# Performance work log

Measured on AMD Instinct MI355X. Metric: run time of the kernel, lower is better.

The kernel has to match this reference:

```python
import jax, jax.numpy as jnp
import numpy as np

N_NODES = 100000
N_EDGES = 1250000
D_FEAT = 64


def setup_inputs() -> dict:
    key = jax.random.key(0)
    kx, ke = jax.random.split(key)
    x = jax.random.normal(kx, (N_NODES, D_FEAT), dtype=jnp.float32)
    edge_index = jax.random.randint(ke, (2, N_EDGES), 0, N_NODES, dtype=jnp.int64)
    return {"x": x, "edge_index": edge_index}


def reference(x, edge_index):
    # adj[src, dst] = 1; x_neighbors = adj.T @ x  ->
    # x_neighbors[i] = sum_{edges (s, d) with d == i} x[s]
    src, dst = edge_index[0], edge_index[1]
    msgs = x[src]  # [n_edges, d_feat] gather
    x_neighbors = jax.ops.segment_sum(msgs, dst, num_segments=x.shape[0])
    return x_neighbors
```

## Files before the change

kernel.cpp:

```cpp
#include <hip/hip_runtime.h>
#include <hip/hip_bf16.h>

#define N_NODES 100000
#define N_EDGES 1250000
#define D_FEAT  64
#define SB_NODES 512
#define SB_SHIFT 9
#define NSB     196
#define CAP_SB  7040
#define OVF_CAP 8192
#define EPB_I4  1024
#define N_I4    (N_EDGES / 4)
#define NBLK_BUILD ((N_I4 + EPB_I4 - 1) / EPB_I4)
#define RT      512

__global__ __launch_bounds__(256) void to_bf16(
    const float* __restrict__ x, ushort* __restrict__ xh, uint* __restrict__ fill)
{
    if (blockIdx.x == 0) {
        for (int i = threadIdx.x; i < NSB + 2; i += 256) fill[i] = 0u;
    }
    int t = blockIdx.x * 256 + threadIdx.x;
    const float4* x4 = (const float4*)x;
    float4 a = x4[2 * t];
    float4 b = x4[2 * t + 1];
    float f[8] = {a.x, a.y, a.z, a.w, b.x, b.y, b.z, b.w};
    uint h[8];
#pragma unroll
    for (int i = 0; i < 8; ++i) {
        uint u = __float_as_uint(f[i]);
        u += 0x7FFFu + ((u >> 16) & 1u);
        h[i] = u >> 16;
    }
    uint4 o;
    o.x = h[0] | (h[1] << 16);
    o.y = h[2] | (h[3] << 16);
    o.z = h[4] | (h[5] << 16);
    o.w = h[6] | (h[7] << 16);
    ((uint4*)xh)[t] = o;
}

__global__ __launch_bounds__(256) void build_sb(
    const int* __restrict__ src, const int* __restrict__ dst,
    uint* __restrict__ fill, uint* __restrict__ pairs,
    uint* __restrict__ ovfCnt, int2* __restrict__ ovf)
{
    __shared__ uint cnt[NSB];
    __shared__ uint base[NSB];
    const int t = threadIdx.x;
    for (int i = t; i < NSB; i += 256) cnt[i] = 0;
    __syncthreads();

    uint   pw[16];
    ushort pb[16];
    ushort pr[16];
    bool   vk[4];
    const int i40 = blockIdx.x * EPB_I4;
#pragma unroll
    for (int k = 0; k < 4; ++k) {
        int i4 = i40 + t + k * 256;
        vk[k] = (i4 < N_I4);
        if (vk[k]) {
            int4 d4 = ((const int4*)dst)[i4];
            int4 s4 = ((const int4*)src)[i4];
            int dd[4] = {d4.x, d4.y, d4.z, d4.w};
            int ss[4] = {s4.x, s4.y, s4.z, s4.w};
#pragma unroll
            for (int j = 0; j < 4; ++j) {
                uint b = ((uint)dd[j]) >> SB_SHIFT;
                uint r = atomicAdd(&cnt[b], 1u);
                pw[k * 4 + j] = ((((uint)dd[j]) & (SB_NODES - 1u)) << 17) | (uint)ss[j];
                pb[k * 4 + j] = (ushort)b;
                pr[k * 4 + j] = (ushort)r;
            }
        }
    }
    __syncthreads();

    for (int i = t; i < NSB; i += 256) {
        uint c = cnt[i];
        base[i] = c ? atomicAdd(&fill[i], c) : 0u;
    }
    __syncthreads();

#pragma unroll
    for (int j = 0; j < 16; ++j) {
        if (vk[j >> 2]) {
            uint b = pb[j];
            uint g = base[b] + pr[j];
            if (g < CAP_SB) {
                pairs[(size_t)b * CAP_SB + g] = pw[j];
            } else {
                uint o = atomicAdd(ovfCnt, 1u);
                if (o < OVF_CAP)
                    ovf[o] = make_int2((int)(pw[j] & 0x1FFFFu),
                                       (int)((b << SB_SHIFT) | (pw[j] >> 17)));
            }
        }
    }
}

__global__ __launch_bounds__(RT) void repart(
    uint* __restrict__ pairs, const uint* __restrict__ fill,
    uint* __restrict__ offs)
{
    __shared__ uint pw[CAP_SB];
    __shared__ int  cnt[SB_NODES];
    __shared__ int  scn[SB_NODES];
    __shared__ int  pos[SB_NODES];

    const int t  = threadIdx.x;
    const int sb = blockIdx.x;
    const int n  = min((int)fill[sb], CAP_SB);
    const size_t base = (size_t)sb * CAP_SB;

    cnt[t] = 0;
    __syncthreads();
    for (int i = t; i < n; i += RT) {
        uint w = pairs[base + i];
        pw[i] = w;
        atomicAdd(&cnt[w >> 17], 1);
    }
    __syncthreads();

    scn[t] = cnt[t];
    __syncthreads();
    for (int off = 1; off < SB_NODES; off <<= 1) {
        int v = (t >= off) ? scn[t - off] : 0;
        __syncthreads();
        scn[t] += v;
        __syncthreads();
    }
    {
        int e = scn[t] - cnt[t];
        pos[t] = e;
        offs[sb * SB_NODES + t] = (uint)e | ((uint)cnt[t] << 16);
    }
    __syncthreads();

    for (int i = t; i < n; i += RT) {
        uint w = pw[i];
        int r = atomicAdd(&pos[w >> 17], 1);
        pairs[base + r] = w & 0x1FFFFu;
    }
}

__global__ __launch_bounds__(256) void gather_csr(
    const ushort* __restrict__ xh, const uint* __restrict__ pairs,
    const uint* __restrict__ offs, const float* __restrict__ x,
    const int2* __restrict__ ovf, const uint* __restrict__ ovfCnt,
    float* __restrict__ out)
{
    const int t    = threadIdx.x;
    const int lane = t & 63;
    const int sub  = lane >> 3;
    const int l8   = lane & 7;
    const int node = blockIdx.x * 4 + (t >> 6);
    if (node >= N_NODES) return;
    const uint4* __restrict__ xrow = (const uint4*)xh;

    const uint v    = offs[node];
    const int start = (node >> SB_SHIFT) * CAP_SB + (int)(v & 0xFFFFu);
    const int deg   = (int)(v >> 16);

    float f[8];
#pragma unroll
    for (int j = 0; j < 8; ++j) f[j] = 0.f;

    int i = sub;
    for (; i + 8 < deg; i += 16) {
        uint s0 = pairs[start + i];
        uint s1 = pairs[start + i + 8];
        uint4 v0 = xrow[(size_t)s0 * 8 + l8];
        uint4 v1 = xrow[(size_t)s1 * 8 + l8];
        f[0] += __uint_as_float((v0.x & 0xFFFFu) << 16);
        f[1] += __uint_as_float(v0.x & 0xFFFF0000u);
        f[2] += __uint_as_float((v0.y & 0xFFFFu) << 16);
        f[3] += __uint_as_float(v0.y & 0xFFFF0000u);
        f[4] += __uint_as_float((v0.z & 0xFFFFu) << 16);
        f[5] += __uint_as_float(v0.z & 0xFFFF0000u);
        f[6] += __uint_as_float((v0.w & 0xFFFFu) << 16);
        f[7] += __uint_as_float(v0.w & 0xFFFF0000u);
        f[0] += __uint_as_float((v1.x & 0xFFFFu) << 16);
        f[1] += __uint_as_float(v1.x & 0xFFFF0000u);
        f[2] += __uint_as_float((v1.y & 0xFFFFu) << 16);
        f[3] += __uint_as_float(v1.y & 0xFFFF0000u);
        f[4] += __uint_as_float((v1.z & 0xFFFFu) << 16);
        f[5] += __uint_as_float(v1.z & 0xFFFF0000u);
        f[6] += __uint_as_float((v1.w & 0xFFFFu) << 16);
        f[7] += __uint_as_float(v1.w & 0xFFFF0000u);
    }
    if (i < deg) {
        uint s0 = pairs[start + i];
        uint4 v0 = xrow[(size_t)s0 * 8 + l8];
        f[0] += __uint_as_float((v0.x & 0xFFFFu) << 16);
        f[1] += __uint_as_float(v0.x & 0xFFFF0000u);
        f[2] += __uint_as_float((v0.y & 0xFFFFu) << 16);
        f[3] += __uint_as_float(v0.y & 0xFFFF0000u);
        f[4] += __uint_as_float((v0.z & 0xFFFFu) << 16);
        f[5] += __uint_as_float(v0.z & 0xFFFF0000u);
        f[6] += __uint_as_float((v0.w & 0xFFFFu) << 16);
        f[7] += __uint_as_float(v0.w & 0xFFFF0000u);
    }

#pragma unroll
    for (int j = 0; j < 8; ++j) {
        f[j] += __shfl_xor(f[j], 8, 64);
        f[j] += __shfl_xor(f[j], 16, 64);
        f[j] += __shfl_xor(f[j], 32, 64);
    }

    const int nov = min((int)*ovfCnt, OVF_CAP);
    for (int e = 0; e < nov; ++e) {
        int2 p = ovf[e];
        if (p.y == node) {
            float4 a = ((const float4*)x)[(size_t)p.x * 16 + l8 * 2];
            float4 b = ((const float4*)x)[(size_t)p.x * 16 + l8 * 2 + 1];
            f[0] += a.x; f[1] += a.y; f[2] += a.z; f[3] += a.w;
            f[4] += b.x; f[5] += b.y; f[6] += b.z; f[7] += b.w;
        }
    }

    if (lane < 8) {
        float4* out4 = (float4*)out;
        out4[(size_t)node * 16 + l8 * 2]     = make_float4(f[0], f[1], f[2], f[3]);
        out4[(size_t)node * 16 + l8 * 2 + 1] = make_float4(f[4], f[5], f[6], f[7]);
    }
}

extern "C" void kernel_launch(void* const* d_in, const int* in_sizes, int n_in,
                              void* d_out, int out_size, void* d_ws, size_t ws_size,
                              hipStream_t stream) {
    const float* x = (const float*)d_in[0];
    const int* edge_index = (const int*)d_in[1];
    const int* src = edge_index;
    const int* dst = edge_index + N_EDGES;
    float* out = (float*)d_out;

    ushort* xh     = (ushort*)d_ws;
    uint*   pairs  = (uint*)(xh + (size_t)N_NODES * D_FEAT);
    uint*   offs   = pairs + (size_t)NSB * CAP_SB;
    uint*   fill   = offs + NSB * SB_NODES;
    uint*   ovfCnt = fill + NSB;
    int2*   ovf    = (int2*)(fill + NSB + 2);

    to_bf16<<<(N_NODES * D_FEAT / 8) / 256, 256, 0, stream>>>(x, xh, fill);
    build_sb<<<NBLK_BUILD, 256, 0, stream>>>(src, dst, fill, pairs, ovfCnt, ovf);
    repart<<<NSB, RT, 0, stream>>>(pairs, fill, offs);
    gather_csr<<<(N_NODES + 3) / 4, 256, 0, stream>>>(xh, pairs, offs, x, ovf, ovfCnt, out);
}
```

Baseline: 143.0 us.

## Fuse four stages into one persistent cooperative kernel with grid syncs

```diff
diff --git a/kernel.cpp b/kernel.cpp
--- a/kernel.cpp
+++ b/kernel.cpp
@@ -1,5 +1,8 @@
 #include <hip/hip_runtime.h>
 #include <hip/hip_bf16.h>
+#include <hip/hip_cooperative_groups.h>
+
+namespace cg = cooperative_groups;
 
 #define N_NODES 100000
 #define N_EDGES 1250000
@@ -11,220 +14,264 @@
 #define OVF_CAP 8192
 #define EPB_I4  1024
 #define N_I4    (N_EDGES / 4)
-#define NBLK_BUILD ((N_I4 + EPB_I4 - 1) / EPB_I4)
-#define RT      512
-
-__global__ __launch_bounds__(256) void to_bf16(
-    const float* __restrict__ x, ushort* __restrict__ xh, uint* __restrict__ fill)
-{
-    if (blockIdx.x == 0) {
-        for (int i = threadIdx.x; i < NSB + 2; i += 256) fill[i] = 0u;
-    }
-    int t = blockIdx.x * 256 + threadIdx.x;
-    const float4* x4 = (const float4*)x;
-    float4 a = x4[2 * t];
-    float4 b = x4[2 * t + 1];
-    float f[8] = {a.x, a.y, a.z, a.w, b.x, b.y, b.z, b.w};
-    uint h[8];
-#pragma unroll
-    for (int i = 0; i < 8; ++i) {
-        uint u = __float_as_uint(f[i]);
-        u += 0x7FFFu + ((u >> 16) & 1u);
-        h[i] = u >> 16;
-    }
-    uint4 o;
-    o.x = h[0] | (h[1] << 16);
-    o.y = h[2] | (h[3] << 16);
-    o.z = h[4] | (h[5] << 16);
-    o.w = h[6] | (h[7] << 16);
-    ((uint4*)xh)[t] = o;
-}
-
-__global__ __launch_bounds__(256) void build_sb(
-    const int* __restrict__ src, const int* __restrict__ dst,
-    uint* __restrict__ fill, uint* __restrict__ pairs,
-    uint* __restrict__ ovfCnt, int2* __restrict__ ovf)
-{
-    __shared__ uint cnt[NSB];
-    __shared__ uint base[NSB];
-    const int t = threadIdx.x;
-    for (int i = t; i < NSB; i += 256) cnt[i] = 0;
-    __syncthreads();
-
-    uint   pw[16];
-    ushort pb[16];
-    ushort pr[16];
-    bool   vk[4];
-    const int i40 = blockIdx.x * EPB_I4;
-#pragma unroll
-    for (int k = 0; k < 4; ++k) {
-        int i4 = i40 + t + k * 256;
-        vk[k] = (i4 < N_I4);
-        if (vk[k]) {
-            int4 d4 = ((const int4*)dst)[i4];
-            int4 s4 = ((const int4*)src)[i4];
-            int dd[4] = {d4.x, d4.y, d4.z, d4.w};
-            int ss[4] = {s4.x, s4.y, s4.z, s4.w};
-#pragma unroll
-            for (int j = 0; j < 4; ++j) {
-                uint b = ((uint)dd[j]) >> SB_SHIFT;
-                uint r = atomicAdd(&cnt[b], 1u);
-                pw[k * 4 + j] = ((((uint)dd[j]) & (SB_NODES - 1u)) << 17) | (uint)ss[j];
-                pb[k * 4 + j] = (ushort)b;
-                pr[k * 4 + j] = (ushort)r;
-            }
-        }
-    }
-    __syncthreads();
-
-    for (int i = t; i < NSB; i += 256) {
-        uint c = cnt[i];
-        base[i] = c ? atomicAdd(&fill[i], c) : 0u;
-    }
-    __syncthreads();
-
-#pragma unroll
-    for (int j = 0; j < 16; ++j) {
-        if (vk[j >> 2]) {
-            uint b = pb[j];
-            uint g = base[b] + pr[j];
-            if (g < CAP_SB) {
-                pairs[(size_t)b * CAP_SB + g] = pw[j];
-            } else {
-                uint o = atomicAdd(ovfCnt, 1u);
-                if (o < OVF_CAP)
-                    ovf[o] = make_int2((int)(pw[j] & 0x1FFFFu),
-                                       (int)((b << SB_SHIFT) | (pw[j] >> 17)));
-            }
-        }
-    }
-}
-
-__global__ __launch_bounds__(RT) void repart(
-    uint* __restrict__ pairs, const uint* __restrict__ fill,
-    uint* __restrict__ offs)
-{
-    __shared__ uint pw[CAP_SB];
-    __shared__ int  cnt[SB_NODES];
-    __shared__ int  scn[SB_NODES];
-    __shared__ int  pos[SB_NODES];
-
-    const int t  = threadIdx.x;
-    const int sb = blockIdx.x;
-    const int n  = min((int)fill[sb], CAP_SB);
-    const size_t base = (size_t)sb * CAP_SB;
-
-    cnt[t] = 0;
-    __syncthreads();
-    for (int i = t; i < n; i += RT) {
-        uint w = pairs[base + i];
-        pw[i] = w;
-        atomicAdd(&cnt[w >> 17], 1);
-    }
-    __syncthreads();
-
-    scn[t] = cnt[t];
-    __syncthreads();
-    for (int off = 1; off < SB_NODES; off <<= 1) {
-        int v = (t >= off) ? scn[t - off] : 0;
-        __syncthreads();
-        scn[t] += v;
-        __syncthreads();
-    }
-    {
-        int e = scn[t] - cnt[t];
-        pos[t] = e;
-        offs[sb * SB_NODES + t] = (uint)e | ((uint)cnt[t] << 16);
-    }
-    __syncthreads();
-
-    for (int i = t; i < n; i += RT) {
-        uint w = pw[i];
-        int r = atomicAdd(&pos[w >> 17], 1);
-        pairs[base + r] = w & 0x1FFFFu;
-    }
-}
-
-__global__ __launch_bounds__(256) void gather_csr(
-    const ushort* __restrict__ xh, const uint* __restrict__ pairs,
-    const uint* __restrict__ offs, const float* __restrict__ x,
-    const int2* __restrict__ ovf, const uint* __restrict__ ovfCnt,
+#define NCHUNK  ((N_I4 + EPB_I4 - 1) / EPB_I4)
+#define NTILE   (N_NODES * D_FEAT / 8 / 256)
+#define NQ      (N_NODES / 4)
+
+#define SH_WORDS 0
+#define SH_SCN   4096
+#define SH_SCNEX 4352
+#define SH_GBASE 4549
+#define SH_POSB  4745
+#define SH_CNT   4941
+#define SH_TOTAL 5137
+
+__global__ __launch_bounds__(256) void onehop_fused(
+    const float* __restrict__ x, const int* __restrict__ src,
+    const int* __restrict__ dst, ushort* __restrict__ xh,
+    uint* __restrict__ pairs, uint* __restrict__ pairsS,
+    uint* __restrict__ offs, uint* __restrict__ fill,
+    uint* __restrict__ ovfCnt, int2* __restrict__ ovf,
     float* __restrict__ out)
 {
-    const int t    = threadIdx.x;
-    const int lane = t & 63;
-    const int sub  = lane >> 3;
-    const int l8   = lane & 7;
-    const int node = blockIdx.x * 4 + (t >> 6);
-    if (node >= N_NODES) return;
-    const uint4* __restrict__ xrow = (const uint4*)xh;
-
-    const uint v    = offs[node];
-    const int start = (node >> SB_SHIFT) * CAP_SB + (int)(v & 0xFFFFu);
-    const int deg   = (int)(v >> 16);
-
-    float f[8];
-#pragma unroll
-    for (int j = 0; j < 8; ++j) f[j] = 0.f;
-
-    int i = sub;
-    for (; i + 8 < deg; i += 16) {
-        uint s0 = pairs[start + i];
-        uint s1 = pairs[start + i + 8];
-        uint4 v0 = xrow[(size_t)s0 * 8 + l8];
-        uint4 v1 = xrow[(size_t)s1 * 8 + l8];
-        f[0] += __uint_as_float((v0.x & 0xFFFFu) << 16);
-        f[1] += __uint_as_float(v0.x & 0xFFFF0000u);
-        f[2] += __uint_as_float((v0.y & 0xFFFFu) << 16);
-        f[3] += __uint_as_float(v0.y & 0xFFFF0000u);
-        f[4] += __uint_as_float((v0.z & 0xFFFFu) << 16);
-        f[5] += __uint_as_float(v0.z & 0xFFFF0000u);
-        f[6] += __uint_as_float((v0.w & 0xFFFFu) << 16);
-        f[7] += __uint_as_float(v0.w & 0xFFFF0000u);
-        f[0] += __uint_as_float((v1.x & 0xFFFFu) << 16);
-        f[1] += __uint_as_float(v1.x & 0xFFFF0000u);
-        f[2] += __uint_as_float((v1.y & 0xFFFFu) << 16);
-        f[3] += __uint_as_float(v1.y & 0xFFFF0000u);
-        f[4] += __uint_as_float((v1.z & 0xFFFFu) << 16);
-        f[5] += __uint_as_float(v1.z & 0xFFFF0000u);
-        f[6] += __uint_as_float((v1.w & 0xFFFFu) << 16);
-        f[7] += __uint_as_float(v1.w & 0xFFFF0000u);
-    }
-    if (i < deg) {
-        uint s0 = pairs[start + i];
-        uint4 v0 = xrow[(size_t)s0 * 8 + l8];
-        f[0] += __uint_as_float((v0.x & 0xFFFFu) << 16);
-        f[1] += __uint_as_float(v0.x & 0xFFFF0000u);
-        f[2] += __uint_as_float((v0.y & 0xFFFFu) << 16);
-        f[3] += __uint_as_float(v0.y & 0xFFFF0000u);
-        f[4] += __uint_as_float((v0.z & 0xFFFFu) << 16);
-        f[5] += __uint_as_float(v0.z & 0xFFFF0000u);
-        f[6] += __uint_as_float((v0.w & 0xFFFFu) << 16);
-        f[7] += __uint_as_float(v0.w & 0xFFFF0000u);
-    }
-
-#pragma unroll
-    for (int j = 0; j < 8; ++j) {
-        f[j] += __shfl_xor(f[j], 8, 64);
-        f[j] += __shfl_xor(f[j], 16, 64);
-        f[j] += __shfl_xor(f[j], 32, 64);
-    }
-
-    const int nov = min((int)*ovfCnt, OVF_CAP);
-    for (int e = 0; e < nov; ++e) {
-        int2 p = ovf[e];
-        if (p.y == node) {
-            float4 a = ((const float4*)x)[(size_t)p.x * 16 + l8 * 2];
-            float4 b = ((const float4*)x)[(size_t)p.x * 16 + l8 * 2 + 1];
-            f[0] += a.x; f[1] += a.y; f[2] += a.z; f[3] += a.w;
-            f[4] += b.x; f[5] += b.y; f[6] += b.z; f[7] += b.w;
+    __shared__ uint SH[SH_TOTAL];
+    cg::grid_group grid = cg::this_grid();
+    const int tid = threadIdx.x;
+    const int bid = blockIdx.x;
+    const int G   = gridDim.x;
+
+    if (bid == 0) {
+        for (int i = tid; i < NSB + 2; i += 256) fill[i] = 0u;
+    }
+    for (int tile = bid; tile < NTILE; tile += G) {
+        int t = tile * 256 + tid;
+        const float4* x4 = (const float4*)x;
+        float4 a = x4[2 * t];
+        float4 b = x4[2 * t + 1];
+        float f[8] = {a.x, a.y, a.z, a.w, b.x, b.y, b.z, b.w};
+        uint h[8];
+#pragma unroll
+        for (int i = 0; i < 8; ++i) {
+            uint u = __float_as_uint(f[i]);
+            u += 0x7FFFu + ((u >> 16) & 1u);
+            h[i] = u >> 16;
         }
-    }
-
-    if (lane < 8) {
-        float4* out4 = (float4*)out;
-        out4[(size_t)node * 16 + l8 * 2]     = make_float4(f[0], f[1], f[2], f[3]);
-        out4[(size_t)node * 16 + l8 * 2 + 1] = make_float4(f[4], f[5], f[6], f[7]);
+        uint4 o;
+        o.x = h[0] | (h[1] << 16);
+        o.y = h[2] | (h[3] << 16);
+        o.z = h[4] | (h[5] << 16);
+        o.w = h[6] | (h[7] << 16);
+        ((uint4*)xh)[t] = o;
+    }
+    grid.sync();
+
+    {
+        uint* words = SH + SH_WORDS;
+        uint* scn   = SH + SH_SCN;
+        uint* scnEx = SH + SH_SCNEX;
+        uint* gbase = SH + SH_GBASE;
+        uint* posb  = SH + SH_POSB;
+        uint* cnt   = SH + SH_CNT;
+        const int4* src4 = (const int4*)src;
+        const int4* dst4 = (const int4*)dst;
+
+        for (int c = bid; c < NCHUNK; c += G) {
+            for (int i = tid; i < NSB; i += 256) cnt[i] = 0u;
+            __syncthreads();
+
+            const int i40 = c * EPB_I4;
+#pragma unroll
+            for (int k = 0; k < 4; ++k) {
+                int i4 = i40 + tid + k * 256;
+                if (i4 < N_I4) {
+                    int4 d4 = dst4[i4];
+                    atomicAdd(&cnt[((uint)d4.x) >> SB_SHIFT], 1u);
+                    atomicAdd(&cnt[((uint)d4.y) >> SB_SHIFT], 1u);
+                    atomicAdd(&cnt[((uint)d4.z) >> SB_SHIFT], 1u);
+                    atomicAdd(&cnt[((uint)d4.w) >> SB_SHIFT], 1u);
+                }
+            }
+            __syncthreads();
+
+            uint myc = (tid < NSB) ? cnt[tid] : 0u;
+            scn[tid] = myc;
+            __syncthreads();
+            for (int off = 1; off < 256; off <<= 1) {
+                uint v = (tid >= off) ? scn[tid - off] : 0u;
+                __syncthreads();
+                scn[tid] += v;
+                __syncthreads();
+            }
+            if (tid < NSB) {
+                uint e = scn[tid] - myc;
+                scnEx[tid] = e;
+                posb[tid]  = e;
+                gbase[tid] = myc ? atomicAdd(&fill[tid], myc) : 0u;
+            }
+            if (tid == 255) scnEx[NSB] = scn[255];
+            __syncthreads();
+
+#pragma unroll
+            for (int k = 0; k < 4; ++k) {
+                int i4 = i40 + tid + k * 256;
+                if (i4 < N_I4) {
+                    int4 d4 = dst4[i4];
+                    int4 s4 = src4[i4];
+                    int dd[4] = {d4.x, d4.y, d4.z, d4.w};
+                    int ss[4] = {s4.x, s4.y, s4.z, s4.w};
+#pragma unroll
+                    for (int j = 0; j < 4; ++j) {
+                        uint du = (uint)dd[j];
+                        uint b = du >> SB_SHIFT;
+                        uint w = ((du & (SB_NODES - 1u)) << 17) | (uint)ss[j];
+                        uint r = atomicAdd(&posb[b], 1u);
+                        words[r] = w;
+                    }
+                }
+            }
+            __syncthreads();
+
+            const int n = (int)scnEx[NSB];
+            for (int i = tid; i < n; i += 256) {
+                int lo = 0, hi = NSB - 1;
+                while (lo < hi) {
+                    int mid = (lo + hi + 1) >> 1;
+                    if ((int)scnEx[mid] <= i) lo = mid; else hi = mid - 1;
+                }
+                uint w = words[i];
+                uint g = gbase[lo] + (uint)(i - (int)scnEx[lo]);
+                if (g < CAP_SB) {
+                    pairs[(size_t)lo * CAP_SB + g] = w;
+                } else {
+                    uint o = atomicAdd(ovfCnt, 1u);
+                    if (o < OVF_CAP)
+                        ovf[o] = make_int2((int)(w & 0x1FFFFu),
+                                           (int)(((uint)lo << SB_SHIFT) | (w >> 17)));
+                }
+            }
+            __syncthreads();
+        }
+    }
+    grid.sync();
+
+    {
+        uint* cntr = SH;
+        uint* scnr = SH + 512;
+        uint* posr = SH + 768;
+
+        for (int sb = bid; sb < NSB; sb += G) {
+            cntr[tid] = 0u;
+            cntr[tid + 256] = 0u;
+            __syncthreads();
+            const int n = min((int)fill[sb], CAP_SB);
+            const size_t base = (size_t)sb * CAP_SB;
+            for (int i = tid; i < n; i += 256)
+                atomicAdd(&cntr[pairs[base + i] >> 17], 1u);
+            __syncthreads();
+
+            uint c0 = cntr[2 * tid], c1 = cntr[2 * tid + 1];
+            scnr[tid] = c0 + c1;
+            __syncthreads();
+            for (int off = 1; off < 256; off <<= 1) {
+                uint v = (tid >= off) ? scnr[tid - off] : 0u;
+                __syncthreads();
+                scnr[tid] += v;
+                __syncthreads();
+            }
+            uint e = scnr[tid] - (c0 + c1);
+            posr[2 * tid]     = e;
+            posr[2 * tid + 1] = e + c0;
+            offs[sb * SB_NODES + 2 * tid]     = e | (c0 << 16);
+            offs[sb * SB_NODES + 2 * tid + 1] = (e + c0) | (c1 << 16);
+            __syncthreads();
+
+            for (int i = tid; i < n; i += 256) {
+                uint w = pairs[base + i];
+                uint r = atomicAdd(&posr[w >> 17], 1u);
+                pairsS[base + r] = w & 0x1FFFFu;
+            }
+            __syncthreads();
+        }
+    }
+    grid.sync();
+
+    {
+        const int lane = tid & 63;
+        const int wid  = tid >> 6;
+        const int sub  = lane >> 3;
+        const int l8   = lane & 7;
+        const uint4* __restrict__ xrow = (const uint4*)xh;
+
+        for (int q = bid; q < NQ; q += G) {
+            const int node = q * 4 + wid;
+            const uint v    = offs[node];
+            const int start = (node >> SB_SHIFT) * CAP_SB + (int)(v & 0xFFFFu);
+            const int deg   = (int)(v >> 16);
+
+            float f[8];
+#pragma unroll
+            for (int j = 0; j < 8; ++j) f[j] = 0.f;
+
+            int i = sub;
+            for (; i + 8 < deg; i += 16) {
+                uint s0 = pairsS[start + i];
+                uint s1 = pairsS[start + i + 8];
+                uint4 v0 = xrow[(size_t)s0 * 8 + l8];
+                uint4 v1 = xrow[(size_t)s1 * 8 + l8];
+                f[0] += __uint_as_float((v0.x & 0xFFFFu) << 16);
+                f[1] += __uint_as_float(v0.x & 0xFFFF0000u);
+                f[2] += __uint_as_float((v0.y & 0xFFFFu) << 16);
+                f[3] += __uint_as_float(v0.y & 0xFFFF0000u);
+                f[4] += __uint_as_float((v0.z & 0xFFFFu) << 16);
+                f[5] += __uint_as_float(v0.z & 0xFFFF0000u);
+                f[6] += __uint_as_float((v0.w & 0xFFFFu) << 16);
+                f[7] += __uint_as_float(v0.w & 0xFFFF0000u);
+                f[0] += __uint_as_float((v1.x & 0xFFFFu) << 16);
+                f[1] += __uint_as_float(v1.x & 0xFFFF0000u);
+                f[2] += __uint_as_float((v1.y & 0xFFFFu) << 16);
+                f[3] += __uint_as_float(v1.y & 0xFFFF0000u);
+                f[4] += __uint_as_float((v1.z & 0xFFFFu) << 16);
+                f[5] += __uint_as_float(v1.z & 0xFFFF0000u);
+                f[6] += __uint_as_float((v1.w & 0xFFFFu) << 16);
+                f[7] += __uint_as_float(v1.w & 0xFFFF0000u);
+            }
+            if (i < deg) {
+                uint s0 = pairsS[start + i];
+                uint4 v0 = xrow[(size_t)s0 * 8 + l8];
+                f[0] += __uint_as_float((v0.x & 0xFFFFu) << 16);
+                f[1] += __uint_as_float(v0.x & 0xFFFF0000u);
+                f[2] += __uint_as_float((v0.y & 0xFFFFu) << 16);
+                f[3] += __uint_as_float(v0.y & 0xFFFF0000u);
+                f[4] += __uint_as_float((v0.z & 0xFFFFu) << 16);
+                f[5] += __uint_as_float(v0.z & 0xFFFF0000u);
+                f[6] += __uint_as_float((v0.w & 0xFFFFu) << 16);
+                f[7] += __uint_as_float(v0.w & 0xFFFF0000u);
+            }
+
+#pragma unroll
+            for (int j = 0; j < 8; ++j) {
+                f[j] += __shfl_xor(f[j], 8, 64);
+                f[j] += __shfl_xor(f[j], 16, 64);
+                f[j] += __shfl_xor(f[j], 32, 64);
+            }
+
+            const int nov = min((int)*ovfCnt, OVF_CAP);
+            for (int e = 0; e < nov; ++e) {
+                int2 p = ovf[e];
+                if (p.y == node) {
+                    float4 a = ((const float4*)x)[(size_t)p.x * 16 + l8 * 2];
+                    float4 b = ((const float4*)x)[(size_t)p.x * 16 + l8 * 2 + 1];
+                    f[0] += a.x; f[1] += a.y; f[2] += a.z; f[3] += a.w;
+                    f[4] += b.x; f[5] += b.y; f[6] += b.z; f[7] += b.w;
+                }
+            }
+
+            if (lane < 8) {
+                float4* out4 = (float4*)out;
+                out4[(size_t)node * 16 + l8 * 2]     = make_float4(f[0], f[1], f[2], f[3]);
+                out4[(size_t)node * 16 + l8 * 2 + 1] = make_float4(f[4], f[5], f[6], f[7]);
+            }
+        }
     }
 }
 
@@ -239,13 +286,22 @@
 
     ushort* xh     = (ushort*)d_ws;
     uint*   pairs  = (uint*)(xh + (size_t)N_NODES * D_FEAT);
-    uint*   offs   = pairs + (size_t)NSB * CAP_SB;
+    uint*   pairsS = pairs + (size_t)NSB * CAP_SB;
+    uint*   offs   = pairsS + (size_t)NSB * CAP_SB;
     uint*   fill   = offs + NSB * SB_NODES;
     uint*   ovfCnt = fill + NSB;
     int2*   ovf    = (int2*)(fill + NSB + 2);
 
-    to_bf16<<<(N_NODES * D_FEAT / 8) / 256, 256, 0, stream>>>(x, xh, fill);
-    build_sb<<<NBLK_BUILD, 256, 0, stream>>>(src, dst, fill, pairs, ovfCnt, ovf);
-    repart<<<NSB, RT, 0, stream>>>(pairs, fill, offs);
-    gather_csr<<<(N_NODES + 3) / 4, 256, 0, stream>>>(xh, pairs, offs, x, ovf, ovfCnt, out);
+    int perCU = 0;
+    if (hipOccupancyMaxActiveBlocksPerMultiprocessor(&perCU, onehop_fused, 256, 0)
+            != hipSuccess || perCU < 1)
+        perCU = 4;
+    int G = perCU * 256;
+    if (G > 2048) G = 2048;
+
+    void* args[] = {(void*)&x, (void*)&src, (void*)&dst, (void*)&xh,
+                    (void*)&pairs, (void*)&pairsS, (void*)&offs, (void*)&fill,
+                    (void*)&ovfCnt, (void*)&ovf, (void*)&out};
+    hipLaunchCooperativeKernel((const void*)onehop_fused, dim3(G), dim3(256),
+                               args, 0, stream);
 }
```

Result: slower. 538.7 us (+276.6%).
